# Performance work log

Hardware: AMD Instinct MI355X
Metric: run time of the kernel (lower is better)

## Reference

```python
import jax, jax.numpy as jnp
import numpy as np

D_MODEL = 1024
NUM_HEADS = 16


def setup_inputs() -> dict:
    key = jax.random.key(0)
    ks = jax.random.split(key, 5)
    B, T, d = 2, 2048, D_MODEL
    s = 1.0 / np.sqrt(d)
    return {
        "x": jax.random.normal(ks[0], (B, T, d), dtype=jnp.float32),
        "W_kqv": jax.random.normal(ks[1], (d, 3 * d), dtype=jnp.float32) * s,
        "b_kqv": jax.random.normal(ks[2], (3 * d,), dtype=jnp.float32) * 0.02,
        "W_o": jax.random.normal(ks[3], (d, d), dtype=jnp.float32) * s,
        "b_o": jax.random.normal(ks[4], (d,), dtype=jnp.float32) * 0.02,
    }


def reference(x, W_kqv, b_kqv, W_o, b_o):
    B, T, d = x.shape
    H = NUM_HEADS
    dk = d // H
    kqv = x @ W_kqv + b_kqv                      # [B, T, 3d]
    # source splits as contiguous chunks in order K, Q, V
    K, Q, V = jnp.split(kqv, 3, axis=-1)
    # [B, T, d] -> [B, H, T, dk]
    to_heads = lambda t: t.reshape(B, T, H, dk).transpose(0, 2, 1, 3)
    K, Q, V = to_heads(K), to_heads(Q), to_heads(V)
    scores = jnp.einsum("bhtd,bhsd->bhts", Q, K)  # [B, H, T, T]
    causal = jnp.triu(jnp.ones((T, T), dtype=bool), k=1)
    scores = jnp.where(causal, -jnp.inf, scores)
    attn = jax.nn.softmax(scores / jnp.sqrt(jnp.asarray(dk, x.dtype)), axis=-1)
    out = jnp.einsum("bhts,bhsd->bhtd", attn, V)  # [B, H, T, dk]
    out = out.transpose(0, 2, 1, 3).reshape(B, T, d)
    return out @ W_o + b_o
```

## Files before the change

kernel.cpp:

```cpp
#include <hip/hip_runtime.h>
#include <hip/hip_bf16.h>
#include <stdint.h>
#include <math.h>

using bf16x8 = __attribute__((ext_vector_type(8))) short;
using f32x4  = __attribute__((ext_vector_type(4))) float;
using f32x16 = __attribute__((ext_vector_type(16))) float;

#define NHEAD  16
#define DK     64
#define TSEQ   2048
#define DMODEL 1024
#define MTOT   4096

#define QSCALE 0.18033688011112042f

static __device__ __forceinline__ ushort f2bf(float f) {
  union { float f; uint32_t u; } v; v.f = f;
  return (ushort)((v.u + 0x7FFFu + ((v.u >> 16) & 1u)) >> 16);
}

static __device__ __forceinline__ float bf2f(ushort u) {
  union { uint32_t u; float f; } v; v.u = ((uint32_t)u) << 16;
  return v.f;
}

static __device__ __forceinline__ uint32_t cvtpk_bf16(float lo, float hi) {
  uint32_t r;
  asm("v_cvt_pk_bf16_f32 %0, %1, %2" : "=v"(r) : "v"(lo), "v"(hi));
  return r;
}

static __device__ __forceinline__ void gload_lds16(const ushort* g, ushort* l) {
  typedef __attribute__((address_space(1))) const uint32_t gu32;
  typedef __attribute__((address_space(3))) uint32_t lu32;
  __builtin_amdgcn_global_load_lds((gu32*)g, (lu32*)l, 16, 0, 0);
}

__global__ void cvt_bf16_kernel(const float* __restrict__ in, ushort* __restrict__ out, int n) {
  int i = (blockIdx.x * 256 + threadIdx.x) * 8;
  const int stride = gridDim.x * 256 * 8;
  for (; i < n; i += stride) {
    const float4* p = (const float4*)(in + i);
    float4 a = p[0], b = p[1];
    bf16x8 v;
    v[0]=(short)f2bf(a.x); v[1]=(short)f2bf(a.y); v[2]=(short)f2bf(a.z); v[3]=(short)f2bf(a.w);
    v[4]=(short)f2bf(b.x); v[5]=(short)f2bf(b.y); v[6]=(short)f2bf(b.z); v[7]=(short)f2bf(b.w);
    *(bf16x8*)(out + i) = v;
  }
}

__global__ __launch_bounds__(256) void transpose_cvt_kernel(const float* __restrict__ W,
                                                            ushort* __restrict__ Wt, int K, int N) {
  __shared__ ushort tl[64][66];
  const int n0 = blockIdx.x * 64, k0 = blockIdx.y * 64;
  const int c = threadIdx.x & 63, r0 = threadIdx.x >> 6;
#pragma unroll
  for (int i = 0; i < 64; i += 4)
    tl[i + r0][c] = f2bf(W[(size_t)(k0 + i + r0) * N + n0 + c]);
  __syncthreads();
#pragma unroll
  for (int i = 0; i < 64; i += 4)
    Wt[(size_t)(n0 + i + r0) * K + k0 + c] = tl[c][i + r0];
}

__global__ __launch_bounds__(256) void transpose_v_kernel(const ushort* __restrict__ V,
                                                          ushort* __restrict__ Vt) {
  __shared__ ushort tl[64][66];
  const int bh = blockIdx.y, t0 = blockIdx.x * 64;
  const int c = threadIdx.x & 63, r0 = threadIdx.x >> 6;
  const ushort* Vb = V + (size_t)bh * TSEQ * DK;
  ushort* Vtb = Vt + (size_t)bh * DK * TSEQ;
#pragma unroll
  for (int i = 0; i < 64; i += 4)
    tl[i + r0][c] = Vb[(size_t)(t0 + i + r0) * DK + c];
  __syncthreads();
#pragma unroll
  for (int i = 0; i < 64; i += 4)
    Vtb[(size_t)(i + r0) * TSEQ + t0 + c] = tl[c][i + r0];
}

template <int MODE>
__global__ __launch_bounds__(256, 2)
void gemm_bt_kernel(const ushort* __restrict__ A, const ushort* __restrict__ Bt,
                    const float* __restrict__ bias,
                    ushort* __restrict__ oK, ushort* __restrict__ oQ, ushort* __restrict__ oV,
                    float* __restrict__ oF, int N, int K) {
  __shared__ ushort As[128 * 32];
  __shared__ ushort Bs[128 * 32];
  const int tid = threadIdx.x;
  const int w = tid >> 6, lane = tid & 63;
  const int m0 = blockIdx.y * 128, n0 = blockIdx.x * 128;
  const int wr = (w >> 1) * 64, wc = (w & 1) * 64;

  const int e0 = ((w * 2 + 0) * 64 + lane) * 8;
  const int e1 = ((w * 2 + 1) * 64 + lane) * 8;
  const ushort* pA0 = A  + (size_t)(m0 + (e0 >> 5)) * K + (e0 & 31);
  const ushort* pA1 = A  + (size_t)(m0 + (e1 >> 5)) * K + (e1 & 31);
  const ushort* pB0 = Bt + (size_t)(n0 + (e0 >> 5)) * K + (e0 & 31);
  const ushort* pB1 = Bt + (size_t)(n0 + (e1 >> 5)) * K + (e1 & 31);

  f32x4 acc[4][4];
#pragma unroll
  for (int i = 0; i < 4; i++)
#pragma unroll
    for (int j = 0; j < 4; j++) acc[i][j] = (f32x4){0.f, 0.f, 0.f, 0.f};

  const int aro = (wr + (lane & 15)) * 32 + (lane >> 4) * 8;
  const int bro = (wc + (lane & 15)) * 32 + (lane >> 4) * 8;

  for (int k0 = 0; k0 < K; k0 += 32) {
    __syncthreads();
    gload_lds16(pA0 + k0, &As[e0]);
    gload_lds16(pA1 + k0, &As[e1]);
    gload_lds16(pB0 + k0, &Bs[e0]);
    gload_lds16(pB1 + k0, &Bs[e1]);
    __syncthreads();
    bf16x8 af[4], bfr[4];
#pragma unroll
    for (int i = 0; i < 4; i++) af[i]  = *(const bf16x8*)&As[aro + i * 16 * 32];
#pragma unroll
    for (int j = 0; j < 4; j++) bfr[j] = *(const bf16x8*)&Bs[bro + j * 16 * 32];
#pragma unroll
    for (int i = 0; i < 4; i++)
#pragma unroll
      for (int j = 0; j < 4; j++)
        acc[i][j] = __builtin_amdgcn_mfma_f32_16x16x32_bf16(af[i], bfr[j], acc[i][j], 0, 0, 0);
  }

  const int rbase = m0 + wr + (lane >> 4) * 4;
  const int cbase = n0 + wc + (lane & 15);
#pragma unroll
  for (int i = 0; i < 4; i++) {
#pragma unroll
    for (int j = 0; j < 4; j++) {
      const int gn = cbase + j * 16;
      const float bv = bias[gn];
#pragma unroll
      for (int jj = 0; jj < 4; jj++) {
        const int gm = rbase + i * 16 + jj;
        float val = acc[i][j][jj] + bv;
        if (MODE == 0) {
          const int sel = gn >> 10, cc = gn & 1023;
          const int hh = cc >> 6, dd = cc & 63;
          const int bbx = gm >> 11, t = gm & 2047;
          if (sel == 1) val *= QSCALE;
          ushort* dst = (sel == 0) ? oK : (sel == 1) ? oQ : oV;
          dst[((size_t)((bbx * NHEAD + hh) * TSEQ + t)) * DK + dd] = f2bf(val);
        } else {
          oF[(size_t)gm * N + gn] = val;
        }
      }
    }
  }
}

__global__ __launch_bounds__(256, 4)
void attn_kernel(const ushort* __restrict__ Qb, const ushort* __restrict__ Kb,
                 const ushort* __restrict__ Vtb, ushort* __restrict__ Opart,
                 float2* __restrict__ mlbuf) {
  __shared__ ushort Ks[2][64 * 64];
  __shared__ ushort Vs[2][64 * 64];

  const int bid = blockIdx.x;
  const int xcd = bid & 7, j = bid >> 3;
  const int bh = xcd + 8 * (j >> 5);
  const int qq = j & 31;
  const int qi = 15 - (qq >> 1);
  const int half = qq & 1;
  const int q0 = qi * 128;
  const int tid = threadIdx.x, w = tid >> 6, lane = tid & 63;
  const int l31 = lane & 31, h = lane >> 5;
  const int qrow = q0 + w * 32 + l31;

  const int t_begin = half ? (qi + 1) : 0;
  const int ntp = qi + 1;

  const ushort* Qp = Qb + ((size_t)bh * TSEQ + qrow) * DK;
  bf16x8 qf[4];
#pragma unroll
  for (int c = 0; c < 4; c++)
    qf[c] = *(const bf16x8*)(Qp + c * 16 + h * 8);

  f32x16 oacc0, oacc1;
#pragma unroll
  for (int r = 0; r < 16; r++) { oacc0[r] = 0.f; oacc1[r] = 0.f; }
  float mrun = -INFINITY, lrun = 0.f;

  const int Bl0 = w * 128 + lane, Bl1 = Bl0 + 64;
  const int sr0 = Bl0 >> 3, sc0 = ((Bl0 & 7) ^ (sr0 & 7)) * 8;
  const int sr1 = Bl1 >> 3, sc1 = ((Bl1 & 7) ^ (sr1 & 7)) * 8;
  const ushort* Kp0 = Kb  + (size_t)bh * TSEQ * DK + sr0 * DK + sc0;
  const ushort* Kp1 = Kb  + (size_t)bh * TSEQ * DK + sr1 * DK + sc1;
  const ushort* Vp0 = Vtb + (size_t)bh * DK * TSEQ + sr0 * TSEQ + sc0;
  const ushort* Vp1 = Vtb + (size_t)bh * DK * TSEQ + sr1 * TSEQ + sc1;

  {
    const int s0 = t_begin * 64;
    gload_lds16(Kp0 + s0 * DK, &Ks[0][Bl0 * 8]);
    gload_lds16(Kp1 + s0 * DK, &Ks[0][Bl1 * 8]);
    gload_lds16(Vp0 + s0, &Vs[0][Bl0 * 8]);
    gload_lds16(Vp1 + s0, &Vs[0][Bl1 * 8]);
  }
  asm volatile("s_waitcnt vmcnt(0)" ::: "memory");
  __builtin_amdgcn_s_barrier();

  for (int tt = 0; tt < ntp; tt++) {
    const int s0 = (t_begin + tt) * 64, cur = tt & 1;

    if (tt + 1 < ntp) {
      const int sn = (t_begin + tt + 1) * 64, nb = cur ^ 1;
      gload_lds16(Kp0 + sn * DK, &Ks[nb][Bl0 * 8]);
      gload_lds16(Kp1 + sn * DK, &Ks[nb][Bl1 * 8]);
      gload_lds16(Vp0 + sn, &Vs[nb][Bl0 * 8]);
      gload_lds16(Vp1 + sn, &Vs[nb][Bl1 * 8]);
    }

    const bool active = (s0 <= q0 + w * 32 + 31);
    if (active) {
      f32x16 ps0, ps1;
#pragma unroll
      for (int r = 0; r < 16; r++) { ps0[r] = 0.f; ps1[r] = 0.f; }
      const char* Kbase = (const char*)&Ks[cur][0];
      __builtin_amdgcn_s_setprio(1);
#pragma unroll
      for (int c = 0; c < 4; c++) {
        const int r0 = l31, r1 = 32 + l31;
        bf16x8 kf0 = *(const bf16x8*)(Kbase + r0 * 128 + ((c * 32 + h * 16) ^ ((r0 & 7) << 4)));
        bf16x8 kf1 = *(const bf16x8*)(Kbase + r1 * 128 + ((c * 32 + h * 16) ^ ((r1 & 7) << 4)));
        ps0 = __builtin_amdgcn_mfma_f32_32x32x16_bf16(kf0, qf[c], ps0, 0, 0, 0);
        ps1 = __builtin_amdgcn_mfma_f32_32x32x16_bf16(kf1, qf[c], ps1, 0, 0, 0);
      }
      __builtin_amdgcn_s_setprio(0);

      if (s0 + 63 > q0 + w * 32) {
#pragma unroll
        for (int r = 0; r < 16; r++) {
          const int kv0 = s0 + (r & 3) + 8 * (r >> 2) + 4 * h;
          if (kv0 > qrow)      ps0[r] = -INFINITY;
          if (kv0 + 32 > qrow) ps1[r] = -INFINITY;
        }
      }

      float pm = ps0[0];
#pragma unroll
      for (int r = 1; r < 16; r++) pm = fmaxf(pm, ps0[r]);
#pragma unroll
      for (int r = 0; r < 16; r++) pm = fmaxf(pm, ps1[r]);
      pm = fmaxf(pm, __shfl_xor(pm, 32));

      if (!__all(pm <= mrun + 8.0f)) {
        const float nm = fmaxf(mrun, pm);
        const float scl = exp2f(mrun - nm);
        lrun *= scl;
#pragma unroll
        for (int r = 0; r < 16; r++) { oacc0[r] *= scl; oacc1[r] *= scl; }
        mrun = nm;
      }

#pragma unroll
      for (int r = 0; r < 16; r++) ps0[r] = exp2f(ps0[r] - mrun);
#pragma unroll
      for (int r = 0; r < 16; r++) ps1[r] = exp2f(ps1[r] - mrun);
      float rs = 0.f;
#pragma unroll
      for (int r = 0; r < 16; r++) rs += ps0[r] + ps1[r];
      rs += __shfl_xor(rs, 32);
      lrun += rs;

      uint32_t w0[2][4], w1[2][4];
#pragma unroll
      for (int a = 0; a < 4; a++) {
        w0[0][a] = cvtpk_bf16(ps0[4 * a + 0], ps0[4 * a + 1]);
        w1[0][a] = cvtpk_bf16(ps0[4 * a + 2], ps0[4 * a + 3]);
        w0[1][a] = cvtpk_bf16(ps1[4 * a + 0], ps1[4 * a + 1]);
        w1[1][a] = cvtpk_bf16(ps1[4 * a + 2], ps1[4 * a + 3]);
      }

      const char* Vbase = (const char*)&Vs[cur][0];
#pragma unroll
      for (int s = 0; s < 2; s++) {
#pragma unroll
        for (int u = 0; u < 2; u++) {
          const int t = 2 * s + u;
          const uint32_t sw0 = h ? w0[s][2 * u] : w0[s][2 * u + 1];
          const uint32_t sw1 = h ? w1[s][2 * u] : w1[s][2 * u + 1];
          const uint32_t rx0 = (uint32_t)__shfl_xor((int)sw0, 32);
          const uint32_t rx1 = (uint32_t)__shfl_xor((int)sw1, 32);
          int4 pw;
          pw.x = h ? (int)rx0 : (int)w0[s][2 * u];
          pw.y = h ? (int)rx1 : (int)w1[s][2 * u];
          pw.z = h ? (int)w0[s][2 * u + 1] : (int)rx0;
          pw.w = h ? (int)w1[s][2 * u + 1] : (int)rx1;
          const bf16x8 pf = __builtin_bit_cast(bf16x8, pw);

          const int vr0 = l31, vr1 = 32 + l31;
          bf16x8 vf0 = *(const bf16x8*)(Vbase + vr0 * 128 + ((t * 32 + h * 16) ^ ((vr0 & 7) << 4)));
          bf16x8 vf1 = *(const bf16x8*)(Vbase + vr1 * 128 + ((t * 32 + h * 16) ^ ((vr1 & 7) << 4)));
          __builtin_amdgcn_s_setprio(1);
          oacc0 = __builtin_amdgcn_mfma_f32_32x32x16_bf16(vf0, pf, oacc0, 0, 0, 0);
          oacc1 = __builtin_amdgcn_mfma_f32_32x32x16_bf16(vf1, pf, oacc1, 0, 0, 0);
          __builtin_amdgcn_s_setprio(0);
        }
      }
    }

    asm volatile("s_waitcnt vmcnt(0)" ::: "memory");
    __builtin_amdgcn_s_barrier();
  }

  const size_t rowidx = ((size_t)bh * TSEQ + qrow) * 2 + half;
  ushort* orow = Opart + rowidx * 64;
#pragma unroll
  for (int r = 0; r < 16; r += 2) {
    const int d0 = (r & 3) + 8 * (r >> 2) + 4 * h;
    const uint32_t v0 = (uint32_t)f2bf(oacc0[r]) | ((uint32_t)f2bf(oacc0[r + 1]) << 16);
    const uint32_t v1 = (uint32_t)f2bf(oacc1[r]) | ((uint32_t)f2bf(oacc1[r + 1]) << 16);
    *(uint32_t*)(orow + d0)      = v0;
    *(uint32_t*)(orow + 32 + d0) = v1;
  }
  if (h == 0) mlbuf[rowidx] = make_float2(mrun, lrun);
}

__global__ __launch_bounds__(256) void combine_kernel(const ushort* __restrict__ Opart,
                                                      const float2* __restrict__ mlbuf,
                                                      ushort* __restrict__ AO) {
  const int gid = blockIdx.x * 4 + (threadIdx.x >> 6);
  const int lane = threadIdx.x & 63;
  const int bh = gid >> 11, q = gid & 2047;
  const float2 a = mlbuf[(size_t)gid * 2 + 0];
  const float2 b = mlbuf[(size_t)gid * 2 + 1];
  const float M = fmaxf(a.x, b.x);
  const float wA = exp2f(a.x - M), wB = exp2f(b.x - M);
  const float inv = 1.f / (wA * a.y + wB * b.y);
  const float va = bf2f(Opart[(size_t)gid * 128 + lane]);
  const float vb = bf2f(Opart[(size_t)gid * 128 + 64 + lane]);
  const float val = (wA * va + wB * vb) * inv;
  const int bb = bh >> 4, hd = bh & 15;
  AO[((size_t)bb * TSEQ + q) * DMODEL + hd * DK + lane] = f2bf(val);
}

extern "C" void kernel_launch(void* const* d_in, const int* in_sizes, int n_in,
                              void* d_out, int out_size, void* d_ws, size_t ws_size,
                              hipStream_t stream) {
  (void)in_sizes; (void)n_in; (void)out_size; (void)ws_size;
  const float* x    = (const float*)d_in[0];
  const float* Wkqv = (const float*)d_in[1];
  const float* bkqv = (const float*)d_in[2];
  const float* Wo   = (const float*)d_in[3];
  const float* bo   = (const float*)d_in[4];
  float* out = (float*)d_out;

  char* ws = (char*)d_ws;
  const size_t MB = 1024 * 1024;
  ushort* x_bf   = (ushort*)(ws + 0);
  ushort* wkqv_t = (ushort*)(ws + 8 * MB);
  ushort* wo_t   = (ushort*)(ws + 14 * MB);
  ushort* Kbuf   = (ushort*)(ws + 16 * MB);
  ushort* Qbuf   = (ushort*)(ws + 24 * MB);
  ushort* Vbuf   = (ushort*)(ws + 32 * MB);
  ushort* Vtbuf  = (ushort*)(ws + 40 * MB);
  ushort* AObuf  = (ushort*)(ws + 48 * MB);
  ushort* Opart  = (ushort*)(ws + 56 * MB);
  float2* mlbuf  = (float2*)(ws + 72 * MB);

  cvt_bf16_kernel<<<2048, 256, 0, stream>>>(x, x_bf, MTOT * DMODEL);
  transpose_cvt_kernel<<<dim3(3072 / 64, 1024 / 64), 256, 0, stream>>>(Wkqv, wkqv_t, 1024, 3072);
  transpose_cvt_kernel<<<dim3(1024 / 64, 1024 / 64), 256, 0, stream>>>(Wo, wo_t, 1024, 1024);
  gemm_bt_kernel<0><<<dim3(3072 / 128, 4096 / 128), 256, 0, stream>>>(
      x_bf, wkqv_t, bkqv, Kbuf, Qbuf, Vbuf, nullptr, 3072, 1024);
  transpose_v_kernel<<<dim3(TSEQ / 64, 32), 256, 0, stream>>>(Vbuf, Vtbuf);
  attn_kernel<<<1024, 256, 0, stream>>>(Qbuf, Kbuf, Vtbuf, Opart, mlbuf);
  combine_kernel<<<16384, 256, 0, stream>>>(Opart, mlbuf, AObuf);
  gemm_bt_kernel<1><<<dim3(1024 / 128, 4096 / 128), 256, 0, stream>>>(
      AObuf, wo_t, bo, nullptr, nullptr, nullptr, out, 1024, 1024);
}
```

Before: 216.7 us.

## Split causal attention KV range into fixed 8-tile chunks with variable partials

Replaces the two-way split of each query tile's key range with chunks of at most 8 KV tiles (64 rows each), so later query tiles get up to 4 partials and the grid grows from 1024 to 1280 blocks with better-balanced work. The combine kernel now merges a variable number of partials per row using their max/sum statistics. The partial buffer layout is reindexed per (head, query tile, part), and the ml buffer moves to make room. The GEMM launch bound also rises to 3 waves per SIMD, trading registers for occupancy, with some risk of spills.

```diff
diff --git a/kernel.cpp b/kernel.cpp
--- a/kernel.cpp
+++ b/kernel.cpp
@@ -81,7 +81,7 @@
 }
 
 template <int MODE>
-__global__ __launch_bounds__(256, 2)
+__global__ __launch_bounds__(256, 3)
 void gemm_bt_kernel(const ushort* __restrict__ A, const ushort* __restrict__ Bt,
                     const float* __restrict__ bias,
                     ushort* __restrict__ oK, ushort* __restrict__ oQ, ushort* __restrict__ oV,
@@ -163,18 +163,22 @@
   __shared__ ushort Vs[2][64 * 64];
 
   const int bid = blockIdx.x;
-  const int xcd = bid & 7, j = bid >> 3;
-  const int bh = xcd + 8 * (j >> 5);
-  const int qq = j & 31;
-  const int qi = 15 - (qq >> 1);
-  const int half = qq & 1;
+  const int xcd = bid & 7, i = bid >> 3;
+  const int bh = xcd + 8 * (i / 40);
+  const int jj = 39 - (i % 40);
+  int qi, p;
+  if (jj < 4)       { qi = jj;                 p = 0; }
+  else if (jj < 12) { int t = jj - 4;  qi = 4  + (t >> 1); p = t & 1; }
+  else if (jj < 24) { int t = jj - 12; qi = 8  + t / 3;    p = t % 3; }
+  else              { int t = jj - 24; qi = 12 + (t >> 2); p = t & 3; }
+
   const int q0 = qi * 128;
   const int tid = threadIdx.x, w = tid >> 6, lane = tid & 63;
   const int l31 = lane & 31, h = lane >> 5;
   const int qrow = q0 + w * 32 + l31;
 
-  const int t_begin = half ? (qi + 1) : 0;
-  const int ntp = qi + 1;
+  const int t_begin = p * 8;
+  const int ntp = min(t_begin + 8, 2 * qi + 2) - t_begin;
 
   const ushort* Qp = Qb + ((size_t)bh * TSEQ + qrow) * DK;
   bf16x8 qf[4];
@@ -309,8 +313,9 @@
     __builtin_amdgcn_s_barrier();
   }
 
-  const size_t rowidx = ((size_t)bh * TSEQ + qrow) * 2 + half;
-  ushort* orow = Opart + rowidx * 64;
+  const int partIdx = (bh * 16 + qi) * 4 + p;
+  const size_t rowslot = (size_t)partIdx * 128 + (qrow & 127);
+  ushort* orow = Opart + rowslot * 64;
 #pragma unroll
   for (int r = 0; r < 16; r += 2) {
     const int d0 = (r & 3) + 8 * (r >> 2) + 4 * h;
@@ -319,7 +324,7 @@
     *(uint32_t*)(orow + d0)      = v0;
     *(uint32_t*)(orow + 32 + d0) = v1;
   }
-  if (h == 0) mlbuf[rowidx] = make_float2(mrun, lrun);
+  if (h == 0) mlbuf[rowslot] = make_float2(mrun, lrun);
 }
 
 __global__ __launch_bounds__(256) void combine_kernel(const ushort* __restrict__ Opart,
@@ -328,14 +333,19 @@
   const int gid = blockIdx.x * 4 + (threadIdx.x >> 6);
   const int lane = threadIdx.x & 63;
   const int bh = gid >> 11, q = gid & 2047;
-  const float2 a = mlbuf[(size_t)gid * 2 + 0];
-  const float2 b = mlbuf[(size_t)gid * 2 + 1];
-  const float M = fmaxf(a.x, b.x);
-  const float wA = exp2f(a.x - M), wB = exp2f(b.x - M);
-  const float inv = 1.f / (wA * a.y + wB * b.y);
-  const float va = bf2f(Opart[(size_t)gid * 128 + lane]);
-  const float vb = bf2f(Opart[(size_t)gid * 128 + 64 + lane]);
-  const float val = (wA * va + wB * vb) * inv;
+  const int qi = q >> 7, np = (qi >> 2) + 1;
+  const size_t base = ((size_t)(bh * 16 + qi) * 4) * 128 + (q & 127);
+
+  float M = -INFINITY;
+  for (int p = 0; p < np; p++) M = fmaxf(M, mlbuf[base + (size_t)p * 128].x);
+  float den = 0.f, acc = 0.f;
+  for (int p = 0; p < np; p++) {
+    const float2 ml = mlbuf[base + (size_t)p * 128];
+    const float wp = exp2f(ml.x - M);
+    den += wp * ml.y;
+    acc += wp * bf2f(Opart[(base + (size_t)p * 128) * 64 + lane]);
+  }
+  const float val = acc / den;
   const int bb = bh >> 4, hd = bh & 15;
   AO[((size_t)bb * TSEQ + q) * DMODEL + hd * DK + lane] = f2bf(val);
 }
@@ -362,7 +372,7 @@
   ushort* Vtbuf  = (ushort*)(ws + 40 * MB);
   ushort* AObuf  = (ushort*)(ws + 48 * MB);
   ushort* Opart  = (ushort*)(ws + 56 * MB);
-  float2* mlbuf  = (float2*)(ws + 72 * MB);
+  float2* mlbuf  = (float2*)(ws + 88 * MB);
 
   cvt_bf16_kernel<<<2048, 256, 0, stream>>>(x, x_bf, MTOT * DMODEL);
   transpose_cvt_kernel<<<dim3(3072 / 64, 1024 / 64), 256, 0, stream>>>(Wkqv, wkqv_t, 1024, 3072);
@@ -370,7 +380,7 @@
   gemm_bt_kernel<0><<<dim3(3072 / 128, 4096 / 128), 256, 0, stream>>>(
       x_bf, wkqv_t, bkqv, Kbuf, Qbuf, Vbuf, nullptr, 3072, 1024);
   transpose_v_kernel<<<dim3(TSEQ / 64, 32), 256, 0, stream>>>(Vbuf, Vtbuf);
-  attn_kernel<<<1024, 256, 0, stream>>>(Qbuf, Kbuf, Vtbuf, Opart, mlbuf);
+  attn_kernel<<<1280, 256, 0, stream>>>(Qbuf, Kbuf, Vtbuf, Opart, mlbuf);
   combine_kernel<<<16384, 256, 0, stream>>>(Opart, mlbuf, AObuf);
   gemm_bt_kernel<1><<<dim3(1024 / 128, 4096 / 128), 256, 0, stream>>>(
       AObuf, wo_t, bo, nullptr, nullptr, nullptr, out, 1024, 1024);
```

Result: no change. 215.5 us (-0.5%).
